# Kernel tuning notes

Hardware: AMD Instinct MI355X
Metric: run time of the kernel (lower is better)

Reference implementation:

```python
import jax, jax.numpy as jnp
import numpy as np

N_HEADS = 8
NS = 4  # samples per point


def _ref_grid(H, W):
    # matches torch: pts[i,j] = ((i+0.5)/(H-1), (j+0.5)/(W-1)) * 2 - 1  -> (y, x)
    ys = ((jnp.arange(H, dtype=jnp.float32) + 0.5) / (H - 1)) * 2.0 - 1.0
    xs = ((jnp.arange(W, dtype=jnp.float32) + 0.5) / (W - 1)) * 2.0 - 1.0
    ref = jnp.stack(jnp.meshgrid(ys, xs, indexing='ij'), axis=-1)  # [H,W,2]
    return ref.reshape(H * W, 2)


def _bilinear_sample(img_flat, yx, H, W):
    # img_flat: [D, H*W], yx: [L, n, 2] normalized (y,x) in [-1,1]
    # grid_sample(mode='bilinear', padding_mode='zeros', align_corners=True)
    y = (yx[..., 0] + 1.0) * 0.5 * (H - 1)
    x = (yx[..., 1] + 1.0) * 0.5 * (W - 1)
    y0 = jnp.floor(y)
    x0 = jnp.floor(x)
    out = jnp.zeros((img_flat.shape[0],) + y.shape, dtype=img_flat.dtype)
    for dy in (0.0, 1.0):
        for dx in (0.0, 1.0):
            yi = y0 + dy
            xi = x0 + dx
            w = (1.0 - jnp.abs(y - yi)) * (1.0 - jnp.abs(x - xi))
            valid = (yi >= 0) & (yi < H) & (xi >= 0) & (xi < W)
            yc = jnp.clip(yi, 0, H - 1).astype(jnp.int32)
            xc = jnp.clip(xi, 0, W - 1).astype(jnp.int32)
            idx = yc * W + xc  # [L,n]
            vals = jnp.take(img_flat, idx.reshape(-1), axis=1).reshape(
                img_flat.shape[0], *idx.shape)  # [D,L,n]
            out = out + vals * jnp.where(valid, w, 0.0)[None]
    return out  # [D,L,n]


def setup_inputs() -> dict:
    key = jax.random.key(0)
    ks = jax.random.split(key, 9)
    B, C, H, W = 8, 256, 64, 64
    A, N = N_HEADS, NS
    x = jax.random.normal(ks[0], (B, C, H, W), dtype=jnp.float32)
    w_att = jax.random.normal(ks[1], (A * N, C), dtype=jnp.float32) * 0.02
    b_att = jnp.zeros((A * N,), dtype=jnp.float32)
    w_off = jax.random.normal(ks[2], (A * N * 2, C), dtype=jnp.float32) * 0.01
    b_off = jax.random.normal(ks[3], (A * N * 2,), dtype=jnp.float32) * 0.1
    w_v = jax.random.normal(ks[4], (C, C), dtype=jnp.float32) * 0.02
    b_v = jnp.zeros((C,), dtype=jnp.float32)
    w_out = jax.random.normal(ks[5], (C, C), dtype=jnp.float32) * 0.02
    b_out = jnp.zeros((C,), dtype=jnp.float32)
    return {"x": x, "w_att": w_att, "b_att": b_att, "w_off": w_off,
            "b_off": b_off, "w_v": w_v, "b_v": b_v, "w_out": w_out,
            "b_out": b_out}


def reference(x, w_att, b_att, w_off, b_off, w_v, b_v, w_out, b_out):
    B, C, H, W = x.shape
    A, N = N_HEADS, NS
    D = C // A
    L = H * W
    xl = x.reshape(B, C, L).transpose(0, 2, 1)  # [B,L,C]
    attn = jax.nn.softmax((xl @ w_att.T + b_att).reshape(B, L, A, N), axis=-1)
    off = (xl @ w_off.T + b_off).reshape(B, L, A, N, 2)
    ref = _ref_grid(H, W)  # [L,2] (y,x)
    pos = ref[None, :, None, None, :] + off  # [B,L,A,N,2]
    pos = pos.transpose(0, 2, 1, 3, 4).reshape(B * A, L, N, 2)
    v = jnp.einsum('bchw,oc->bohw', x, w_v) + b_v[None, :, None, None]
    v_flat = v.reshape(B * A, D, L)
    samp = jax.vmap(lambda im, g: _bilinear_sample(im, g, H, W))(v_flat, pos)  # [BA,D,L,N]
    attn_ = attn.transpose(0, 2, 1, 3).reshape(B * A, L, N)
    agg = (samp * attn_[:, None]).sum(axis=3)  # [BA,D,L]
    v2 = agg.reshape(B, A * D, H, W)
    y = jnp.einsum('bchw,oc->bohw', v2, w_out) + b_out[None, :, None, None]
    return y
```

## Files before the change

### kernel.cpp

```cpp
#include <hip/hip_runtime.h>
#include <math.h>
#include <stdint.h>

#define BQ 8
#define CC 256
#define HH 64
#define WW 64
#define LL 4096
#define AH 8
#define DD 32

typedef __attribute__((ext_vector_type(4))) float f32x4;
typedef __attribute__((ext_vector_type(8))) short short8;

__device__ __forceinline__ uint32_t pk_bf16(float a, float b) {
    uint32_t r;
    asm("v_cvt_pk_bf16_f32 %0, %1, %2" : "=v"(r) : "v"(a), "v"(b));
    return r;
}
__device__ __forceinline__ float bf_lo(uint32_t u) { return __uint_as_float(u << 16); }
__device__ __forceinline__ float bf_hi(uint32_t u) { return __uint_as_float(u & 0xffff0000u); }

__device__ __forceinline__ void split2(float a, float b, uint32_t& hi, uint32_t& lo) {
    hi = pk_bf16(a, b);
    float ah = bf_lo(hi), bh = bf_hi(hi);
    lo = pk_bf16(a - ah, b - bh);
}


__device__ __forceinline__ void load8(float4 v[8], const float* p, size_t stride) {
#pragma unroll
    for (int i = 0; i < 8; ++i) v[i] = *(const float4*)(p + (size_t)i * stride);
}

__device__ __forceinline__ void writeA(const float4 av[8], uint32_t* as, int a_r0, int a_f4) {
#pragma unroll
    for (int i = 0; i < 8; ++i) {
        int r = a_r0 + i * 16;
        uint32_t lo = pk_bf16(av[i].x, av[i].y);
        uint32_t hi = pk_bf16(av[i].z, av[i].w);
        int slot = (a_f4 >> 1) ^ (r & 7);
        *(uint2*)&as[r * 32 + (slot << 2) + ((a_f4 & 1) << 1)] = make_uint2(lo, hi);
    }
}

__device__ __forceinline__ void writeB_x(const float4 bv[8], uint32_t* bs, int b_kb, int b_l0) {
#pragma unroll
    for (int j = 0; j < 4; ++j) {
        int l = b_l0 * 4 + j;
        uint32_t w0 = pk_bf16(((const float*)&bv[0])[j], ((const float*)&bv[1])[j]);
        uint32_t w1 = pk_bf16(((const float*)&bv[2])[j], ((const float*)&bv[3])[j]);
        uint32_t w2 = pk_bf16(((const float*)&bv[4])[j], ((const float*)&bv[5])[j]);
        uint32_t w3 = pk_bf16(((const float*)&bv[6])[j], ((const float*)&bv[7])[j]);
        int slot = b_kb ^ (l & 7);
        *(uint4*)&bs[l * 32 + (slot << 2)] = make_uint4(w0, w1, w2, w3);
    }
}

__device__ __forceinline__ void compute_tile(const uint32_t* as, const uint32_t* bs,
                                             f32x4 acc[4][4], int lane, int wm, int wn) {
#pragma unroll
    for (int ks = 0; ks < 2; ++ks) {
        int ag = ks * 4 + (lane >> 4);
        short8 af[4], bf[4];
#pragma unroll
        for (int mf = 0; mf < 4; ++mf) {
            int r = wm * 64 + mf * 16 + (lane & 15);
            af[mf] = *(const short8*)&as[r * 32 + ((ag ^ (r & 7)) << 2)];
        }
#pragma unroll
        for (int nf = 0; nf < 4; ++nf) {
            int r = wn * 64 + nf * 16 + (lane & 15);
            bf[nf] = *(const short8*)&bs[r * 32 + ((ag ^ (r & 7)) << 2)];
        }
#pragma unroll
        for (int mf = 0; mf < 4; ++mf)
#pragma unroll
            for (int nf = 0; nf < 4; ++nf)
                acc[mf][nf] = __builtin_amdgcn_mfma_f32_16x16x32_bf16(
                    af[mf], bf[nf], acc[mf][nf], 0, 0, 0);
    }
}

union ProjSmem {
    struct { uint32_t a[2][128 * 32]; uint32_t b[2][128 * 32]; } v;
    struct { uint32_t ah[2][96 * 32]; uint32_t al[2][96 * 32];
             uint32_t bh[2][64 * 32]; uint32_t bl[2][64 * 32]; } ao;
};

__global__ __launch_bounds__(256, 2)
void gemm_proj(const float* __restrict__ X,
               const float* __restrict__ w_v, const float* __restrict__ b_v,
               const float* __restrict__ w_att, const float* __restrict__ w_off,
               const float* __restrict__ b_att, const float* __restrict__ b_off,
               uint16_t* __restrict__ vout, float* __restrict__ logits)
{
    __shared__ ProjSmem sm;

    const int bid = blockIdx.x;
    const int t  = threadIdx.x;
    const int lane = t & 63;
    const int wv = t >> 6;
    const int wm = wv >> 1, wn = wv & 1;

    if (bid < 512) {
        const int nb = bid & 255;
        const int b  = nb >> 5;
        const int lb = nb & 31;
        const int ob = bid >> 8;

        const int a_f4 = t & 15, a_r0 = t >> 4;
        const int b_kb = t & 7,  b_l0 = t >> 3;

        const float* Ap = w_v + (size_t)(ob * 128 + a_r0) * CC + a_f4 * 4;
        const float* Bp = X + ((size_t)b * CC + b_kb * 8) * LL + lb * 128 + b_l0 * 4;

        f32x4 acc[4][4];
#pragma unroll
        for (int i = 0; i < 4; ++i)
#pragma unroll
            for (int j = 0; j < 4; ++j) acc[i][j] = (f32x4)0.0f;

        float4 av[8], bv[8];
        load8(av, Ap, (size_t)16 * CC);
        load8(bv, Bp, (size_t)LL);
        writeA(av, sm.v.a[0], a_r0, a_f4);
        writeB_x(bv, sm.v.b[0], b_kb, b_l0);
        __syncthreads();

        for (int kc = 0; kc < 4; ++kc) {
            const int cur = kc & 1;
            if (kc < 3) {
                load8(av, Ap + (kc + 1) * 64, (size_t)16 * CC);
                load8(bv, Bp + (size_t)(kc + 1) * 64 * LL, (size_t)LL);
            }
            compute_tile(sm.v.a[cur], sm.v.b[cur], acc, lane, wm, wn);
            if (kc < 3) {
                writeA(av, sm.v.a[cur ^ 1], a_r0, a_f4);
                writeB_x(bv, sm.v.b[cur ^ 1], b_kb, b_l0);
                __syncthreads();
            }
        }

        const int l_base = lb * 128 + wn * 64 + (lane & 15);
        const int o_base = ob * 128 + wm * 64 + ((lane >> 4) << 2);
#pragma unroll
        for (int mf = 0; mf < 4; ++mf) {
            int o0 = o_base + mf * 16;
            float4 bs = *(const float4*)(b_v + o0);
            int a_h = o0 >> 5;
            int d0 = o0 & 31;
#pragma unroll
            for (int nf = 0; nf < 4; ++nf) {
                int l = l_base + nf * 16;
                uint32_t p0 = pk_bf16(acc[mf][nf][0] + bs.x, acc[mf][nf][1] + bs.y);
                uint32_t p1 = pk_bf16(acc[mf][nf][2] + bs.z, acc[mf][nf][3] + bs.w);
                *(uint2*)(vout + ((size_t)(b * AH + a_h) * LL + l) * DD + d0) =
                    make_uint2(p0, p1);
            }
        }
        return;
    }

    {
        const int r2 = bid - 512;
        const int lb = r2 & 63;
        const int b  = r2 >> 6;

        const int tr   = t >> 4;
        const int a_f4 = t & 15;
        const int b_kb = t & 7;
        const int b_l0 = t >> 3;

        const float* Bp = X + ((size_t)b * CC + b_kb * 8) * LL + lb * 64 + b_l0 * 2;

        f32x4 acc[3][2];
#pragma unroll
        for (int i = 0; i < 3; ++i)
#pragma unroll
            for (int j = 0; j < 2; ++j) acc[i][j] = (f32x4)0.0f;

        float4 av[6];
        float2 bv[8];

        auto loadT = [&](int kc) {
#pragma unroll
            for (int i = 0; i < 6; ++i) {
                int r = i * 16 + tr;
                const float* wp = (i < 2) ? (w_att + (size_t)r * CC)
                                          : (w_off + (size_t)(r - 32) * CC);
                av[i] = *(const float4*)(wp + kc * 64 + a_f4 * 4);
            }
#pragma unroll
            for (int m = 0; m < 8; ++m)
                bv[m] = *(const float2*)(Bp + (size_t)(kc * 64 + m) * LL);
        };

        auto writeT = [&](int buf) {
#pragma unroll
            for (int i = 0; i < 6; ++i) {
                int r = i * 16 + tr;
                uint32_t h0, q0, h1, q1;
                split2(av[i].x, av[i].y, h0, q0);
                split2(av[i].z, av[i].w, h1, q1);
                int idx = r * 32 + (((a_f4 >> 1) ^ (r & 7)) << 2) + ((a_f4 & 1) << 1);
                *(uint2*)&sm.ao.ah[buf][idx] = make_uint2(h0, h1);
                *(uint2*)&sm.ao.al[buf][idx] = make_uint2(q0, q1);
            }
#pragma unroll
            for (int j = 0; j < 2; ++j) {
                int l = b_l0 * 2 + j;
                uint32_t h[4], q[4];
#pragma unroll
                for (int p = 0; p < 4; ++p) {
                    float e0 = j ? bv[2 * p].y     : bv[2 * p].x;
                    float e1 = j ? bv[2 * p + 1].y : bv[2 * p + 1].x;
                    split2(e0, e1, h[p], q[p]);
                }
                int idx = l * 32 + ((b_kb ^ (l & 7)) << 2);
                *(uint4*)&sm.ao.bh[buf][idx] = make_uint4(h[0], h[1], h[2], h[3]);
                *(uint4*)&sm.ao.bl[buf][idx] = make_uint4(q[0], q[1], q[2], q[3]);
            }
        };

        auto computeT = [&](int buf) {
#pragma unroll
            for (int ks = 0; ks < 2; ++ks) {
                int ag = ks * 4 + (lane >> 4);
                short8 afh[3], afl[3], bfh[2], bfl[2];
#pragma unroll
                for (int mf = 0; mf < 3; ++mf) {
                    int r = wm * 48 + mf * 16 + (lane & 15);
                    int off = r * 32 + ((ag ^ (r & 7)) << 2);
                    afh[mf] = *(const short8*)&sm.ao.ah[buf][off];
                    afl[mf] = *(const short8*)&sm.ao.al[buf][off];
                }
#pragma unroll
                for (int nf = 0; nf < 2; ++nf) {
                    int r = wn * 32 + nf * 16 + (lane & 15);
                    int off = r * 32 + ((ag ^ (r & 7)) << 2);
                    bfh[nf] = *(const short8*)&sm.ao.bh[buf][off];
                    bfl[nf] = *(const short8*)&sm.ao.bl[buf][off];
                }
#pragma unroll
                for (int mf = 0; mf < 3; ++mf)
#pragma unroll
                    for (int nf = 0; nf < 2; ++nf) {
                        acc[mf][nf] = __builtin_amdgcn_mfma_f32_16x16x32_bf16(
                            afh[mf], bfh[nf], acc[mf][nf], 0, 0, 0);
                        acc[mf][nf] = __builtin_amdgcn_mfma_f32_16x16x32_bf16(
                            afh[mf], bfl[nf], acc[mf][nf], 0, 0, 0);
                        acc[mf][nf] = __builtin_amdgcn_mfma_f32_16x16x32_bf16(
                            afl[mf], bfh[nf], acc[mf][nf], 0, 0, 0);
                    }
            }
        };

        loadT(0);
        writeT(0);
        __syncthreads();
        for (int kc = 0; kc < 4; ++kc) {
            const int cur = kc & 1;
            if (kc < 3) loadT(kc + 1);
            computeT(cur);
            if (kc < 3) { writeT(cur ^ 1); __syncthreads(); }
        }

        const int l_base = lb * 64 + wn * 32 + (lane & 15);
        const int o_base = wm * 48 + ((lane >> 4) << 2);
#pragma unroll
        for (int mf = 0; mf < 3; ++mf) {
            int o0 = o_base + mf * 16;
            const float* bp = (o0 < 32) ? (b_att + o0) : (b_off + (o0 - 32));
            float4 bs = *(const float4*)bp;
#pragma unroll
            for (int nf = 0; nf < 2; ++nf) {
                int l = l_base + nf * 16;
                float* op = logits + ((size_t)b * 96 + o0) * LL + l;
                op[(size_t)0 * LL] = acc[mf][nf][0] + bs.x;
                op[(size_t)1 * LL] = acc[mf][nf][1] + bs.y;
                op[(size_t)2 * LL] = acc[mf][nf][2] + bs.z;
                op[(size_t)3 * LL] = acc[mf][nf][3] + bs.w;
            }
        }
    }
}

__global__ __launch_bounds__(256, 2)
void gemm_out(const uint16_t* __restrict__ Agg, const float* __restrict__ Wm,
              const float* __restrict__ bias, float* __restrict__ out)
{
    __shared__ uint32_t a_s[2][128 * 32];
    __shared__ uint32_t b_s[2][128 * 32];

    const int nb = blockIdx.x;
    const int b  = nb >> 5;
    const int lb = nb & 31;
    const int ob = blockIdx.y;
    const int t  = threadIdx.x;
    const int lane = t & 63;
    const int wv = t >> 6;
    const int wm = wv >> 1, wn = wv & 1;

    const int a_f4 = t & 15, a_r0 = t >> 4;
    const int br = t >> 1;
    const int bh = t & 1;

    const float* Ap = Wm + (size_t)(ob * 128 + a_r0) * CC + a_f4 * 4;
    const uint16_t* Bp = Agg + ((size_t)b * LL + lb * 128 + br) * CC + bh * 32;

    f32x4 acc[4][4];
#pragma unroll
    for (int i = 0; i < 4; ++i)
#pragma unroll
        for (int j = 0; j < 4; ++j) acc[i][j] = (f32x4)0.0f;

    float4 av[8];
    uint4 bq[4];
    load8(av, Ap, (size_t)16 * CC);
#pragma unroll
    for (int j = 0; j < 4; ++j) bq[j] = *(const uint4*)(Bp + j * 8);
    writeA(av, a_s[0], a_r0, a_f4);
#pragma unroll
    for (int j = 0; j < 4; ++j)
        *(uint4*)&b_s[0][br * 32 + ((((bh << 2) + j) ^ (br & 7)) << 2)] = bq[j];
    __syncthreads();

    for (int kc = 0; kc < 4; ++kc) {
        const int cur = kc & 1;
        if (kc < 3) {
            load8(av, Ap + (kc + 1) * 64, (size_t)16 * CC);
#pragma unroll
            for (int j = 0; j < 4; ++j)
                bq[j] = *(const uint4*)(Bp + (kc + 1) * 64 + j * 8);
        }
        compute_tile(a_s[cur], b_s[cur], acc, lane, wm, wn);
        if (kc < 3) {
            writeA(av, a_s[cur ^ 1], a_r0, a_f4);
#pragma unroll
            for (int j = 0; j < 4; ++j)
                *(uint4*)&b_s[cur ^ 1][br * 32 + ((((bh << 2) + j) ^ (br & 7)) << 2)] = bq[j];
            __syncthreads();
        }
    }

    const int l_base = lb * 128 + wn * 64 + (lane & 15);
    const int o_base = ob * 128 + wm * 64 + ((lane >> 4) << 2);
#pragma unroll
    for (int mf = 0; mf < 4; ++mf) {
        int o0 = o_base + mf * 16;
        float4 bs = *(const float4*)(bias + o0);
#pragma unroll
        for (int nf = 0; nf < 4; ++nf) {
            int l = l_base + nf * 16;
            float* op = out + ((size_t)b * CC + o0) * LL + l;
            op[(size_t)0 * LL] = acc[mf][nf][0] + bs.x;
            op[(size_t)1 * LL] = acc[mf][nf][1] + bs.y;
            op[(size_t)2 * LL] = acc[mf][nf][2] + bs.z;
            op[(size_t)3 * LL] = acc[mf][nf][3] + bs.w;
        }
    }
}

__global__ __launch_bounds__(256)
void sample_kernel(const uint16_t* __restrict__ v_samp,
                   const float* __restrict__ logits,
                   uint16_t* __restrict__ agg)
{
    const int bid  = blockIdx.x;
    const int xcd  = bid & 7;
    const int rest = bid >> 3;
    const int img  = rest >> 6;
    const int lt   = rest & 63;
    const int ba   = xcd * 8 + img;
    const int b = ba >> 3, a = ba & 7;

    const int t  = threadIdx.x;
    const int l  = lt * 64 + (t >> 2);
    const int d0 = (t & 3) * 8;

    const float* la = logits + ((size_t)b * 96 + a * 4) * LL + l;
    float e0 = la[0], e1 = la[(size_t)LL], e2 = la[(size_t)2 * LL], e3 = la[(size_t)3 * LL];
    float m = fmaxf(fmaxf(e0, e1), fmaxf(e2, e3));
    e0 = expf(e0 - m); e1 = expf(e1 - m); e2 = expf(e2 - m); e3 = expf(e3 - m);
    float inv = 1.0f / (e0 + e1 + e2 + e3);
    float attn[4] = {e0 * inv, e1 * inv, e2 * inv, e3 * inv};

    const int gi = l >> 6, gj = l & 63;
    float ry = (gi + 0.5f) * (2.0f / 63.0f) - 1.0f;
    float rx = (gj + 0.5f) * (2.0f / 63.0f) - 1.0f;
    const float* lo = logits + ((size_t)b * 96 + 32 + a * 8) * LL + l;

    int   offs[16];
    float wgt[16];
#pragma unroll
    for (int n = 0; n < 4; ++n) {
        float py = ry + lo[(size_t)(n * 2 + 0) * LL];
        float px = rx + lo[(size_t)(n * 2 + 1) * LL];
        float y = (py + 1.0f) * 0.5f * 63.0f;
        float x = (px + 1.0f) * 0.5f * 63.0f;
        float yf = floorf(y), xf = floorf(x);
        int y0i = (int)yf, x0i = (int)xf;
        float fy = y - yf, fx = x - xf;
        float wts[4] = {(1.f - fy) * (1.f - fx), (1.f - fy) * fx,
                        fy * (1.f - fx),         fy * fx};
#pragma unroll
        for (int c2 = 0; c2 < 4; ++c2) {
            int yi = y0i + (c2 >> 1);
            int xi = x0i + (c2 & 1);
            bool valid = (yi >= 0) & (yi < HH) & (xi >= 0) & (xi < WW);
            int yc = min(max(yi, 0), HH - 1);
            int xc = min(max(xi, 0), WW - 1);
            wgt[n * 4 + c2]  = valid ? attn[n] * wts[c2] : 0.0f;
            offs[n * 4 + c2] = (yc * WW + xc) * DD;
        }
    }

    float acc[8];
#pragma unroll
    for (int q = 0; q < 8; ++q) acc[q] = 0.f;

    const uint16_t* vb = v_samp + (size_t)ba * LL * DD + d0;
#pragma unroll
    for (int g = 0; g < 2; ++g) {
        uint4 rv[8];
#pragma unroll
        for (int i = 0; i < 8; ++i)
            rv[i] = *(const uint4*)(vb + offs[g * 8 + i]);
#pragma unroll
        for (int i = 0; i < 8; ++i) {
            float w = wgt[g * 8 + i];
            acc[0] += w * bf_lo(rv[i].x); acc[1] += w * bf_hi(rv[i].x);
            acc[2] += w * bf_lo(rv[i].y); acc[3] += w * bf_hi(rv[i].y);
            acc[4] += w * bf_lo(rv[i].z); acc[5] += w * bf_hi(rv[i].z);
            acc[6] += w * bf_lo(rv[i].w); acc[7] += w * bf_hi(rv[i].w);
        }
    }

    uint32_t p0 = pk_bf16(acc[0], acc[1]);
    uint32_t p1 = pk_bf16(acc[2], acc[3]);
    uint32_t p2 = pk_bf16(acc[4], acc[5]);
    uint32_t p3 = pk_bf16(acc[6], acc[7]);
    *(uint4*)(agg + ((size_t)b * LL + l) * CC + a * DD + d0) =
        make_uint4(p0, p1, p2, p3);
}

extern "C" void kernel_launch(void* const* d_in, const int* in_sizes, int n_in,
                              void* d_out, int out_size, void* d_ws, size_t ws_size,
                              hipStream_t stream) {
    const float* x     = (const float*)d_in[0];
    const float* w_att = (const float*)d_in[1];
    const float* b_att = (const float*)d_in[2];
    const float* w_off = (const float*)d_in[3];
    const float* b_off = (const float*)d_in[4];
    const float* w_v   = (const float*)d_in[5];
    const float* b_v   = (const float*)d_in[6];
    const float* w_out = (const float*)d_in[7];
    const float* b_out = (const float*)d_in[8];
    float* out = (float*)d_out;

    float* ws      = (float*)d_ws;
    float* logits  = ws;
    uint16_t* agg  = (uint16_t*)(logits + (size_t)BQ * 96 * LL);
    uint16_t* v_samp = (uint16_t*)d_out;

    dim3 blk(256);
    gemm_proj<<<dim3(1024), blk, 0, stream>>>(x, w_v, b_v, w_att, w_off,
                                              b_att, b_off, v_samp, logits);
    sample_kernel<<<dim3(4096), blk, 0, stream>>>(v_samp, logits, agg);
    gemm_out<<<dim3(256, 2), blk, 0, stream>>>(agg, w_out, b_out, out);
}
```

Baseline: 66.95 us.

## Dedupe sampling-weight computation via shared memory and remap GEMM block order

The sample kernel previously made all four threads of a point redo the softmax and bilinear offset/weight math. Now only the first 64 threads compute the 16 offsets and weights per point, store them in padded shared memory, and sync before the gather. This removes the 4x redundant logit loads and transcendental math, at the cost of a block barrier and leaving three wavefronts idle during setup. The projection GEMM interleaves value and attention/offset blocks in groups of 8, and both GEMMs put the batch index in the low bits of blockIdx. The likely aim is to spread work types and batches evenly across XCDs.

```diff
diff --git a/kernel.cpp b/kernel.cpp
--- a/kernel.cpp
+++ b/kernel.cpp
@@ -97,17 +97,18 @@
 {
     __shared__ ProjSmem sm;
 
-    const int bid = blockIdx.x;
+    const int bid  = blockIdx.x;
+    const int type = (bid >> 3) & 1;
+    const int sub  = (bid >> 4) * 8 + (bid & 7);
     const int t  = threadIdx.x;
     const int lane = t & 63;
     const int wv = t >> 6;
     const int wm = wv >> 1, wn = wv & 1;
 
-    if (bid < 512) {
-        const int nb = bid & 255;
-        const int b  = nb >> 5;
-        const int lb = nb & 31;
-        const int ob = bid >> 8;
+    if (type == 0) {
+        const int b  = sub & 7;
+        const int lb = (sub >> 3) & 31;
+        const int ob = sub >> 8;
 
         const int a_f4 = t & 15, a_r0 = t >> 4;
         const int b_kb = t & 7,  b_l0 = t >> 3;
@@ -163,9 +164,8 @@
     }
 
     {
-        const int r2 = bid - 512;
-        const int lb = r2 & 63;
-        const int b  = r2 >> 6;
+        const int b  = sub & 7;
+        const int lb = sub >> 3;
 
         const int tr   = t >> 4;
         const int a_f4 = t & 15;
@@ -293,10 +293,10 @@
     __shared__ uint32_t a_s[2][128 * 32];
     __shared__ uint32_t b_s[2][128 * 32];
 
-    const int nb = blockIdx.x;
-    const int b  = nb >> 5;
-    const int lb = nb & 31;
-    const int ob = blockIdx.y;
+    const int bid = blockIdx.x;
+    const int b  = bid & 7;
+    const int lb = (bid >> 3) & 31;
+    const int ob = bid >> 8;
     const int t  = threadIdx.x;
     const int lane = t & 63;
     const int wv = t >> 6;
@@ -367,6 +367,9 @@
                    const float* __restrict__ logits,
                    uint16_t* __restrict__ agg)
 {
+    __shared__ int   offs_s[64 * 17];
+    __shared__ float wgt_s[64 * 17];
+
     const int bid  = blockIdx.x;
     const int xcd  = bid & 7;
     const int rest = bid >> 3;
@@ -375,46 +378,51 @@
     const int ba   = xcd * 8 + img;
     const int b = ba >> 3, a = ba & 7;
 
-    const int t  = threadIdx.x;
-    const int l  = lt * 64 + (t >> 2);
-    const int d0 = (t & 3) * 8;
-
-    const float* la = logits + ((size_t)b * 96 + a * 4) * LL + l;
-    float e0 = la[0], e1 = la[(size_t)LL], e2 = la[(size_t)2 * LL], e3 = la[(size_t)3 * LL];
-    float m = fmaxf(fmaxf(e0, e1), fmaxf(e2, e3));
-    e0 = expf(e0 - m); e1 = expf(e1 - m); e2 = expf(e2 - m); e3 = expf(e3 - m);
-    float inv = 1.0f / (e0 + e1 + e2 + e3);
-    float attn[4] = {e0 * inv, e1 * inv, e2 * inv, e3 * inv};
-
-    const int gi = l >> 6, gj = l & 63;
-    float ry = (gi + 0.5f) * (2.0f / 63.0f) - 1.0f;
-    float rx = (gj + 0.5f) * (2.0f / 63.0f) - 1.0f;
-    const float* lo = logits + ((size_t)b * 96 + 32 + a * 8) * LL + l;
-
-    int   offs[16];
-    float wgt[16];
-#pragma unroll
-    for (int n = 0; n < 4; ++n) {
-        float py = ry + lo[(size_t)(n * 2 + 0) * LL];
-        float px = rx + lo[(size_t)(n * 2 + 1) * LL];
-        float y = (py + 1.0f) * 0.5f * 63.0f;
-        float x = (px + 1.0f) * 0.5f * 63.0f;
-        float yf = floorf(y), xf = floorf(x);
-        int y0i = (int)yf, x0i = (int)xf;
-        float fy = y - yf, fx = x - xf;
-        float wts[4] = {(1.f - fy) * (1.f - fx), (1.f - fy) * fx,
-                        fy * (1.f - fx),         fy * fx};
-#pragma unroll
-        for (int c2 = 0; c2 < 4; ++c2) {
-            int yi = y0i + (c2 >> 1);
-            int xi = x0i + (c2 & 1);
-            bool valid = (yi >= 0) & (yi < HH) & (xi >= 0) & (xi < WW);
-            int yc = min(max(yi, 0), HH - 1);
-            int xc = min(max(xi, 0), WW - 1);
-            wgt[n * 4 + c2]  = valid ? attn[n] * wts[c2] : 0.0f;
-            offs[n * 4 + c2] = (yc * WW + xc) * DD;
-        }
-    }
+    const int t = threadIdx.x;
+
+    if (t < 64) {
+        const int l = lt * 64 + t;
+        const float* la = logits + ((size_t)b * 96 + a * 4) * LL + l;
+        float e0 = la[0], e1 = la[(size_t)LL], e2 = la[(size_t)2 * LL], e3 = la[(size_t)3 * LL];
+        float m = fmaxf(fmaxf(e0, e1), fmaxf(e2, e3));
+        e0 = expf(e0 - m); e1 = expf(e1 - m); e2 = expf(e2 - m); e3 = expf(e3 - m);
+        float inv = 1.0f / (e0 + e1 + e2 + e3);
+        float attn[4] = {e0 * inv, e1 * inv, e2 * inv, e3 * inv};
+
+        const int gi = l >> 6, gj = l & 63;
+        float ry = (gi + 0.5f) * (2.0f / 63.0f) - 1.0f;
+        float rx = (gj + 0.5f) * (2.0f / 63.0f) - 1.0f;
+        const float* lo = logits + ((size_t)b * 96 + 32 + a * 8) * LL + l;
+
+#pragma unroll
+        for (int n = 0; n < 4; ++n) {
+            float py = ry + lo[(size_t)(n * 2 + 0) * LL];
+            float px = rx + lo[(size_t)(n * 2 + 1) * LL];
+            float y = (py + 1.0f) * 0.5f * 63.0f;
+            float x = (px + 1.0f) * 0.5f * 63.0f;
+            float yf = floorf(y), xf = floorf(x);
+            int y0i = (int)yf, x0i = (int)xf;
+            float fy = y - yf, fx = x - xf;
+            float wts[4] = {(1.f - fy) * (1.f - fx), (1.f - fy) * fx,
+                            fy * (1.f - fx),         fy * fx};
+#pragma unroll
+            for (int c2 = 0; c2 < 4; ++c2) {
+                int yi = y0i + (c2 >> 1);
+                int xi = x0i + (c2 & 1);
+                bool valid = (yi >= 0) & (yi < HH) & (xi >= 0) & (xi < WW);
+                int yc = min(max(yi, 0), HH - 1);
+                int xc = min(max(xi, 0), WW - 1);
+                wgt_s[t * 17 + n * 4 + c2]  = valid ? attn[n] * wts[c2] : 0.0f;
+                offs_s[t * 17 + n * 4 + c2] = (yc * WW + xc) * DD;
+            }
+        }
+    }
+    __syncthreads();
+
+    const int pt = t >> 2;
+    const int cg = t & 3;
+    const int l  = lt * 64 + pt;
+    const int d0 = cg * 8;
 
     float acc[8];
 #pragma unroll
@@ -424,12 +432,16 @@
 #pragma unroll
     for (int g = 0; g < 2; ++g) {
         uint4 rv[8];
-#pragma unroll
-        for (int i = 0; i < 8; ++i)
-            rv[i] = *(const uint4*)(vb + offs[g * 8 + i]);
+        float w8[8];
 #pragma unroll
         for (int i = 0; i < 8; ++i) {
-            float w = wgt[g * 8 + i];
+            int idx = offs_s[pt * 17 + g * 8 + i];
+            w8[i] = wgt_s[pt * 17 + g * 8 + i];
+            rv[i] = *(const uint4*)(vb + idx);
+        }
+#pragma unroll
+        for (int i = 0; i < 8; ++i) {
+            float w = w8[i];
             acc[0] += w * bf_lo(rv[i].x); acc[1] += w * bf_hi(rv[i].x);
             acc[2] += w * bf_lo(rv[i].y); acc[3] += w * bf_hi(rv[i].y);
             acc[4] += w * bf_lo(rv[i].z); acc[5] += w * bf_hi(rv[i].z);
@@ -468,5 +480,5 @@
     gemm_proj<<<dim3(1024), blk, 0, stream>>>(x, w_v, b_v, w_att, w_off,
                                               b_att, b_off, v_samp, logits);
     sample_kernel<<<dim3(4096), blk, 0, stream>>>(v_samp, logits, agg);
-    gemm_out<<<dim3(256, 2), blk, 0, stream>>>(agg, w_out, b_out, out);
-}
+    gemm_out<<<dim3(512), blk, 0, stream>>>(agg, w_out, b_out, out);
+}
```

Result: slower. 69.27 us (+3.5%).
